# Optimization experiments

Measured on AMD Instinct MI355X. Metric: run time of the kernel, lower is better.

Reference implementation:

```python
import jax, jax.numpy as jnp
import numpy as np


def setup_inputs() -> dict:
    key = jax.random.key(0)
    ks = jax.random.split(key, 5)
    B, Lq, Lkv, HQ, H, D, S, BS = 1, 256, 4096, 32, 2, 128, 16, 64
    q = jax.random.normal(ks[0], (B, Lq, HQ, D), jnp.float32)
    k = jax.random.normal(ks[1], (B, Lkv, H, D), jnp.float32)
    v = jax.random.normal(ks[2], (B, Lkv, H, D), jnp.float32)
    w = jax.random.uniform(ks[3], (B, Lq, HQ, S), jnp.float32)
    block_indices = jax.random.randint(ks[4], (B, Lq, H, S), 0, Lkv // BS).astype(jnp.int32)
    return {"q": q, "k": k, "v": v, "w": w, "block_indices": block_indices, "block_size": BS}


def reference(q, k, v, w, block_indices, block_size):
    # q: (B, Lq, HQ, D); k,v: (B, Lkv, H, D); w: (B, Lq, HQ, num_weights);
    # block_indices: (B, Lq, H, S) int32, entries < 0 are skipped.
    B, Lq, HQ, D = q.shape
    H = k.shape[2]
    S = block_indices.shape[-1]
    G = HQ // H  # query heads per kv head
    nb = k.shape[1] // block_size
    sm_scale = 1.0 / (D ** 0.5)  # default scale in the kernel

    # Reshape KV into blocks: (B, H, nb, BS, D)
    kb = k.reshape(B, nb, block_size, H, D).transpose(0, 3, 1, 2, 4)
    vb = v.reshape(B, nb, block_size, H, D).transpose(0, 3, 1, 2, 4)

    idx = block_indices.transpose(0, 2, 1, 3)  # (B, H, Lq, S)
    valid = idx >= 0
    idx = jnp.maximum(idx, 0)

    # Gather selected blocks per (batch, kv_head): -> (B, H, Lq, S, BS, D)
    gather = jax.vmap(jax.vmap(lambda blocks, ind: blocks[ind]))
    kg = gather(kb, idx)
    vg = gather(vb, idx)

    # Group query heads by kv head: (B, H, Lq, G, D)
    qh = q.reshape(B, Lq, H, G, D).transpose(0, 2, 1, 3, 4)

    # Per-block scores and per-block softmax over the BS keys (axis u)
    scores = jnp.einsum('bhlgd,bhlsud->bhlgsu', qh, kg) * sm_scale
    p = jax.nn.softmax(scores, axis=-1)

    # Per-(head, block) learned weight; only first S weights of w are used.
    wh = w[..., :S].reshape(B, Lq, H, G, S).transpose(0, 2, 1, 3, 4)  # (B,H,Lq,G,S)
    coef = wh * valid[:, :, :, None, :].astype(p.dtype)
    p = p * coef[..., None]

    o = jnp.einsum('bhlgsu,bhlsud->bhlgd', p, vg)  # (B, H, Lq, G, D)
    return o.transpose(0, 2, 1, 3, 4).reshape(B, Lq, HQ, D)
```

## Files before the change

kernel.cpp:

```cpp
#include <hip/hip_runtime.h>
#include <hip/hip_bf16.h>


namespace {

constexpr int kLq = 256, kHQ = 32, kH = 2, kG = 16, kD = 128, kS = 16;
constexpr int kNB = 64;
constexpr float kScaleLog2e = 0.08838834764831845f * 1.4426950408889634f;

constexpr int kKPackN = kH * kNB * 16 * 64;
constexpr int kPStr   = 72;
constexpr int kSStr   = 136;

typedef short s16x8 __attribute__((ext_vector_type(8)));
typedef float f32x4 __attribute__((ext_vector_type(4)));

union U32BF2 { unsigned int u; __hip_bfloat162 h; };
union FragU  { uint4 u; s16x8 v; };

static __device__ inline unsigned int pk_bf16(float a, float b) {
    U32BF2 z; z.h = __float22bfloat162_rn(make_float2(a, b));
    return z.u;
}

__global__ __launch_bounds__(256)
void pack_kv(const float* __restrict__ k, const float* __restrict__ v,
             uint4* __restrict__ kp, uint4* __restrict__ vp)
{
    __shared__ unsigned short S_s[32 * kSStr];

    const int bid  = blockIdx.x;
    const int isV  = bid & 1;
    const int half = (bid >> 1) & 1;
    const int blk  = (bid >> 2) & 63;
    const int h    = bid >> 8;
    const int t    = threadIdx.x;
    const int lane = t & 63, n = lane & 15, quad = lane >> 4;
    const int wv   = t >> 6;

    {
        const float* src = (isV ? v : k) +
            ((size_t)(blk * 64 + half * 32) * kH + h) * kD;
        const int r0 = t >> 5, c4 = (t & 31) << 2;
        #pragma unroll
        for (int p = 0; p < 4; ++p) {
            const int r = p * 8 + r0;
            const float4 f = *(const float4*)(src + (size_t)r * (kH * kD) + c4);
            *(unsigned int*)&S_s[r * kSStr + c4]     = pk_bf16(f.x, f.y);
            *(unsigned int*)&S_s[r * kSStr + c4 + 2] = pk_bf16(f.z, f.w);
        }
    }
    __syncthreads();

    const size_t obase = (size_t)(h * 64 + blk) * 16 * 64;
    if (!isV) {
        #pragma unroll
        for (int rep = 0; rep < 2; ++rep) {
            const int cl    = wv * 2 + rep;
            const int t_loc = cl >> 2, st = cl & 3;
            const int c     = (2 * half + t_loc) * 4 + st;
            const int u_loc = t_loc * 16 + n;
            kp[obase + (size_t)c * 64 + lane] =
                *(const uint4*)&S_s[u_loc * kSStr + st * 32 + quad * 8];
        }
    } else {
        #pragma unroll
        for (int rep = 0; rep < 2; ++rep) {
            const int dt = wv * 2 + rep;
            const int c  = dt * 2 + half;
            const int d  = dt * 16 + n;
            unsigned short s[8];
            #pragma unroll
            for (int j = 0; j < 8; ++j) s[j] = S_s[(quad * 8 + j) * kSStr + d];
            uint4 val;
            val.x = s[0] | ((unsigned)s[1] << 16);
            val.y = s[2] | ((unsigned)s[3] << 16);
            val.z = s[4] | ((unsigned)s[5] << 16);
            val.w = s[6] | ((unsigned)s[7] << 16);
            vp[obase + (size_t)c * 64 + lane] = val;
        }
    }
}

__global__ __launch_bounds__(512, 4)
void hsa_main(const float* __restrict__ q, const float* __restrict__ w,
              const int* __restrict__ bidx, const uint4* __restrict__ kp,
              const uint4* __restrict__ vp, float* __restrict__ out)
{
    __shared__ __align__(16) float smem[8192];

    const int bid  = blockIdx.x;
    const int l    = bid >> 1;
    const int h    = bid & 1;
    const int tid  = threadIdx.x;
    const int wave = tid >> 6;
    const int lane = tid & 63;
    const int n    = lane & 15;
    const int quad = lane >> 4;

    s16x8 qf[4];
    {
        const float* qb = q + ((size_t)l * kHQ + h * kG + n) * kD + quad * 8;
        #pragma unroll
        for (int st = 0; st < 4; ++st) {
            const float4 f0 = *(const float4*)(qb + st * 32);
            const float4 f1 = *(const float4*)(qb + st * 32 + 4);
            union { s16x8 v; unsigned int u[4]; } z;
            z.u[0] = pk_bf16(f0.x, f0.y); z.u[1] = pk_bf16(f0.z, f0.w);
            z.u[2] = pk_bf16(f1.x, f1.y); z.u[3] = pk_bf16(f1.z, f1.w);
            qf[st] = z.v;
        }
    }

    int   base2[2];
    float wval2[2];
    #pragma unroll
    for (int j = 0; j < 2; ++j) {
        const int s  = wave * 2 + j;
        const int bi = bidx[(size_t)(l * kH + h) * kS + s];
        wval2[j] = (bi < 0) ? 0.f : w[((size_t)l * kHQ + h * kG + n) * kS + s];
        base2[j] = (h * kNB + max(bi, 0)) * 1024;
    }

    unsigned short* Pw = (unsigned short*)smem + wave * (kG * kPStr);

    FragU kA[4], kB[4], vr[4];
    #pragma unroll
    for (int st = 0; st < 4; ++st) kA[st].u = kp[base2[0] + (0 * 4 + st) * 64 + lane];
    #pragma unroll
    for (int st = 0; st < 4; ++st) kB[st].u = kp[base2[0] + (1 * 4 + st) * 64 + lane];
    #pragma unroll
    for (int i = 0; i < 4; ++i)    vr[i].u  = vp[base2[0] + i * 64 + lane];
    __builtin_amdgcn_sched_barrier(0);

    f32x4 oacc[8];
    #pragma unroll
    for (int dt = 0; dt < 8; ++dt) oacc[dt] = (f32x4){0.f, 0.f, 0.f, 0.f};

    #pragma unroll
    for (int jb = 0; jb < 2; ++jb) {
        float part = 0.f;
        #pragma unroll
        for (int t = 0; t < 4; ++t) {
            FragU* cur = (t & 1) ? kB : kA;
            f32x4 sc = {0.f, 0.f, 0.f, 0.f};
            #pragma unroll
            for (int st = 0; st < 4; ++st)
                sc = __builtin_amdgcn_mfma_f32_16x16x32_bf16(cur[st].v, qf[st], sc, 0, 0, 0);

            if (t < 2) {
                #pragma unroll
                for (int st = 0; st < 4; ++st)
                    cur[st].u = kp[base2[jb] + ((t + 2) * 4 + st) * 64 + lane];
            } else if (jb == 0) {
                #pragma unroll
                for (int st = 0; st < 4; ++st)
                    cur[st].u = kp[base2[1] + ((t - 2) * 4 + st) * 64 + lane];
            }
            __builtin_amdgcn_sched_barrier(0);

            #pragma unroll
            for (int r = 0; r < 4; ++r) {
                sc[r] = exp2f(sc[r] * kScaleLog2e);
                part += sc[r];
            }
            const unsigned long long pq =
                ((unsigned long long)pk_bf16(sc[2], sc[3]) << 32) | pk_bf16(sc[0], sc[1]);
            *(unsigned long long*)&Pw[n * kPStr + t * 16 + quad * 4] = pq;
        }

        part += __shfl_xor(part, 16);
        part += __shfl_xor(part, 32);
        const float coef = wval2[jb] / part;

        const s16x8 bf0 = *(const s16x8*)&Pw[n * kPStr + quad * 8];
        const s16x8 bf1 = *(const s16x8*)&Pw[n * kPStr + 32 + quad * 8];

        const f32x4 zero = {0.f, 0.f, 0.f, 0.f};
        #pragma unroll
        for (int vg = 0; vg < 4; ++vg) {
            const int dt0 = vg * 2;
            f32x4 p0 = __builtin_amdgcn_mfma_f32_16x16x32_bf16(vr[0].v, bf0, zero, 0, 0, 0);
            p0       = __builtin_amdgcn_mfma_f32_16x16x32_bf16(vr[1].v, bf1, p0,   0, 0, 0);
            f32x4 p1 = __builtin_amdgcn_mfma_f32_16x16x32_bf16(vr[2].v, bf0, zero, 0, 0, 0);
            p1       = __builtin_amdgcn_mfma_f32_16x16x32_bf16(vr[3].v, bf1, p1,   0, 0, 0);

            if (vg < 3) {
                #pragma unroll
                for (int i = 0; i < 4; ++i)
                    vr[i].u = vp[base2[jb] + ((vg + 1) * 4 + i) * 64 + lane];
            } else if (jb == 0) {
                #pragma unroll
                for (int i = 0; i < 4; ++i)
                    vr[i].u = vp[base2[1] + i * 64 + lane];
            }
            __builtin_amdgcn_sched_barrier(0);

            #pragma unroll
            for (int r = 0; r < 4; ++r) {
                oacc[dt0 + 0][r] = fmaf(coef, p0[r], oacc[dt0 + 0][r]);
                oacc[dt0 + 1][r] = fmaf(coef, p1[r], oacc[dt0 + 1][r]);
            }
        }
    }

    __syncthreads();
    float* epi = smem;

    if (wave >= 4) {
        #pragma unroll
        for (int dt = 0; dt < 8; ++dt)
            *(f32x4*)&epi[(wave - 4) * 2048 + dt * 256 + lane * 4] = oacc[dt];
    }
    __syncthreads();
    if (wave < 4) {
        #pragma unroll
        for (int dt = 0; dt < 8; ++dt) {
            const f32x4 o = *(const f32x4*)&epi[wave * 2048 + dt * 256 + lane * 4];
            #pragma unroll
            for (int r = 0; r < 4; ++r) oacc[dt][r] += o[r];
        }
    }
    __syncthreads();
    if (wave == 2 || wave == 3) {
        #pragma unroll
        for (int dt = 0; dt < 8; ++dt)
            *(f32x4*)&epi[(wave - 2) * 2048 + dt * 256 + lane * 4] = oacc[dt];
    }
    __syncthreads();
    if (wave < 2) {
        #pragma unroll
        for (int dt = 0; dt < 8; ++dt) {
            const f32x4 o = *(const f32x4*)&epi[wave * 2048 + dt * 256 + lane * 4];
            #pragma unroll
            for (int r = 0; r < 4; ++r) oacc[dt][r] += o[r];
        }
    }
    __syncthreads();
    if (wave == 1) {
        #pragma unroll
        for (int dt = 0; dt < 8; ++dt)
            *(f32x4*)&epi[dt * 256 + lane * 4] = oacc[dt];
    }
    __syncthreads();
    if (wave == 0) {
        float* ob = out + ((size_t)l * kHQ + h * kG + n) * kD;
        #pragma unroll
        for (int dt = 0; dt < 8; ++dt) {
            const f32x4 o = *(const f32x4*)&epi[dt * 256 + lane * 4];
            float4 val;
            #pragma unroll
            for (int r = 0; r < 4; ++r) (&val.x)[r] = oacc[dt][r] + o[r];
            *(float4*)(ob + dt * 16 + quad * 4) = val;
        }
    }
}

}

extern "C" void kernel_launch(void* const* d_in, const int* in_sizes, int n_in,
                              void* d_out, int out_size, void* d_ws, size_t ws_size,
                              hipStream_t stream)
{
    const float* q    = (const float*)d_in[0];
    const float* k    = (const float*)d_in[1];
    const float* v    = (const float*)d_in[2];
    const float* w    = (const float*)d_in[3];
    const int*   bidx = (const int*)d_in[4];
    float* out = (float*)d_out;

    uint4* kp = (uint4*)d_ws;
    uint4* vp = (uint4*)((char*)d_ws + (size_t)kKPackN * 16);

    pack_kv<<<dim3(512), dim3(256), 0, stream>>>(k, v, kp, vp);
    hsa_main<<<dim3(kLq * kH), dim3(512), 0, stream>>>(q, w, bidx, kp, vp, out);
}
```

Before: 89.02 us.

## Interleave two KV blocks' score phases and stage Q fragments in LDS

Each wave now computes QK scores for both of its selected blocks in interleaved order with separate K register buffers, and writes P into two LDS tiles. The PV phases then run back to back. Q fragments move from registers into LDS, which frees VGPRs but adds LDS reads before every MFMA. Shared memory grows to about 68 KB per block, which may cut the number of resident blocks below the launch-bound target of 4.

Result: no change. 88.81 us (-0.2%).

```diff
diff --git a/kernel.cpp b/kernel.cpp
--- a/kernel.cpp
+++ b/kernel.cpp
@@ -11,6 +11,9 @@
 constexpr int kKPackN = kH * kNB * 16 * 64;
 constexpr int kPStr   = 72;
 constexpr int kSStr   = 136;
+
+constexpr int kQOff = 0;
+constexpr int kPOff = 32768;
 
 typedef short s16x8 __attribute__((ext_vector_type(8)));
 typedef float f32x4 __attribute__((ext_vector_type(4)));
@@ -87,7 +90,7 @@
               const int* __restrict__ bidx, const uint4* __restrict__ kp,
               const uint4* __restrict__ vp, float* __restrict__ out)
 {
-    __shared__ __align__(16) float smem[8192];
+    __shared__ __align__(16) unsigned char smem[69632];
 
     const int bid  = blockIdx.x;
     const int l    = bid >> 1;
@@ -98,85 +101,108 @@
     const int n    = lane & 15;
     const int quad = lane >> 4;
 
-    s16x8 qf[4];
+    unsigned char* qlds = smem + kQOff + wave * 4096 + lane * 16;
     {
         const float* qb = q + ((size_t)l * kHQ + h * kG + n) * kD + quad * 8;
         #pragma unroll
         for (int st = 0; st < 4; ++st) {
             const float4 f0 = *(const float4*)(qb + st * 32);
             const float4 f1 = *(const float4*)(qb + st * 32 + 4);
-            union { s16x8 v; unsigned int u[4]; } z;
-            z.u[0] = pk_bf16(f0.x, f0.y); z.u[1] = pk_bf16(f0.z, f0.w);
-            z.u[2] = pk_bf16(f1.x, f1.y); z.u[3] = pk_bf16(f1.z, f1.w);
-            qf[st] = z.v;
-        }
-    }
-
-    int   base2[2];
-    float wval2[2];
-    #pragma unroll
-    for (int j = 0; j < 2; ++j) {
-        const int s  = wave * 2 + j;
-        const int bi = bidx[(size_t)(l * kH + h) * kS + s];
-        wval2[j] = (bi < 0) ? 0.f : w[((size_t)l * kHQ + h * kG + n) * kS + s];
-        base2[j] = (h * kNB + max(bi, 0)) * 1024;
-    }
-
-    unsigned short* Pw = (unsigned short*)smem + wave * (kG * kPStr);
+            uint4 z;
+            z.x = pk_bf16(f0.x, f0.y); z.y = pk_bf16(f0.z, f0.w);
+            z.z = pk_bf16(f1.x, f1.y); z.w = pk_bf16(f1.z, f1.w);
+            *(uint4*)(qlds + st * 1024) = z;
+        }
+    }
+
+    int   baseA, baseB;
+    float wvalA, wvalB;
+    {
+        const int sA = wave * 2, sB = wave * 2 + 1;
+        const int biA = bidx[(size_t)(l * kH + h) * kS + sA];
+        const int biB = bidx[(size_t)(l * kH + h) * kS + sB];
+        wvalA = (biA < 0) ? 0.f : w[((size_t)l * kHQ + h * kG + n) * kS + sA];
+        wvalB = (biB < 0) ? 0.f : w[((size_t)l * kHQ + h * kG + n) * kS + sB];
+        baseA = (h * kNB + max(biA, 0)) * 1024;
+        baseB = (h * kNB + max(biB, 0)) * 1024;
+    }
+
+    unsigned short* PA = (unsigned short*)(smem + kPOff + wave * 4608);
+    unsigned short* PB = PA + kG * kPStr;
 
     FragU kA[4], kB[4], vr[4];
     #pragma unroll
-    for (int st = 0; st < 4; ++st) kA[st].u = kp[base2[0] + (0 * 4 + st) * 64 + lane];
-    #pragma unroll
-    for (int st = 0; st < 4; ++st) kB[st].u = kp[base2[0] + (1 * 4 + st) * 64 + lane];
-    #pragma unroll
-    for (int i = 0; i < 4; ++i)    vr[i].u  = vp[base2[0] + i * 64 + lane];
+    for (int st = 0; st < 4; ++st) kA[st].u = kp[baseA + st * 64 + lane];
+    #pragma unroll
+    for (int st = 0; st < 4; ++st) kB[st].u = kp[baseB + st * 64 + lane];
+    #pragma unroll
+    for (int i = 0; i < 4; ++i)    vr[i].u  = vp[baseA + i * 64 + lane];
     __builtin_amdgcn_sched_barrier(0);
 
     f32x4 oacc[8];
     #pragma unroll
     for (int dt = 0; dt < 8; ++dt) oacc[dt] = (f32x4){0.f, 0.f, 0.f, 0.f};
 
-    #pragma unroll
-    for (int jb = 0; jb < 2; ++jb) {
-        float part = 0.f;
-        #pragma unroll
-        for (int t = 0; t < 4; ++t) {
-            FragU* cur = (t & 1) ? kB : kA;
+    float partA = 0.f, partB = 0.f;
+    #pragma unroll
+    for (int t = 0; t < 4; ++t) {
+        {
             f32x4 sc = {0.f, 0.f, 0.f, 0.f};
             #pragma unroll
-            for (int st = 0; st < 4; ++st)
-                sc = __builtin_amdgcn_mfma_f32_16x16x32_bf16(cur[st].v, qf[st], sc, 0, 0, 0);
-
-            if (t < 2) {
+            for (int st = 0; st < 4; ++st) {
+                const s16x8 aq = *(const s16x8*)(qlds + st * 1024);
+                sc = __builtin_amdgcn_mfma_f32_16x16x32_bf16(kA[st].v, aq, sc, 0, 0, 0);
+            }
+            if (t < 3) {
                 #pragma unroll
                 for (int st = 0; st < 4; ++st)
-                    cur[st].u = kp[base2[jb] + ((t + 2) * 4 + st) * 64 + lane];
-            } else if (jb == 0) {
-                #pragma unroll
-                for (int st = 0; st < 4; ++st)
-                    cur[st].u = kp[base2[1] + ((t - 2) * 4 + st) * 64 + lane];
+                    kA[st].u = kp[baseA + ((t + 1) * 4 + st) * 64 + lane];
             }
             __builtin_amdgcn_sched_barrier(0);
-
             #pragma unroll
             for (int r = 0; r < 4; ++r) {
                 sc[r] = exp2f(sc[r] * kScaleLog2e);
-                part += sc[r];
+                partA += sc[r];
             }
             const unsigned long long pq =
                 ((unsigned long long)pk_bf16(sc[2], sc[3]) << 32) | pk_bf16(sc[0], sc[1]);
-            *(unsigned long long*)&Pw[n * kPStr + t * 16 + quad * 4] = pq;
-        }
-
-        part += __shfl_xor(part, 16);
-        part += __shfl_xor(part, 32);
-        const float coef = wval2[jb] / part;
-
-        const s16x8 bf0 = *(const s16x8*)&Pw[n * kPStr + quad * 8];
-        const s16x8 bf1 = *(const s16x8*)&Pw[n * kPStr + 32 + quad * 8];
-
-        const f32x4 zero = {0.f, 0.f, 0.f, 0.f};
+            *(unsigned long long*)&PA[n * kPStr + t * 16 + quad * 4] = pq;
+        }
+        {
+            f32x4 sc = {0.f, 0.f, 0.f, 0.f};
+            #pragma unroll
+            for (int st = 0; st < 4; ++st) {
+                const s16x8 aq = *(const s16x8*)(qlds + st * 1024);
+                sc = __builtin_amdgcn_mfma_f32_16x16x32_bf16(kB[st].v, aq, sc, 0, 0, 0);
+            }
+            if (t < 3) {
+                #pragma unroll
+                for (int st = 0; st < 4; ++st)
+                    kB[st].u = kp[baseB + ((t + 1) * 4 + st) * 64 + lane];
+            }
+            __builtin_amdgcn_sched_barrier(0);
+            #pragma unroll
+            for (int r = 0; r < 4; ++r) {
+                sc[r] = exp2f(sc[r] * kScaleLog2e);
+                partB += sc[r];
+            }
+            const unsigned long long pq =
+                ((unsigned long long)pk_bf16(sc[2], sc[3]) << 32) | pk_bf16(sc[0], sc[1]);
+            *(unsigned long long*)&PB[n * kPStr + t * 16 + quad * 4] = pq;
+        }
+    }
+
+    partA += __shfl_xor(partA, 16);
+    partA += __shfl_xor(partA, 32);
+    partB += __shfl_xor(partB, 16);
+    partB += __shfl_xor(partB, 32);
+    const float coefA = wvalA / partA;
+    const float coefB = wvalB / partB;
+
+    const f32x4 zero = {0.f, 0.f, 0.f, 0.f};
+    {
+        const s16x8 bf0 = *(const s16x8*)&PA[n * kPStr + quad * 8];
+        const s16x8 bf1 = *(const s16x8*)&PA[n * kPStr + 32 + quad * 8];
         #pragma unroll
         for (int vg = 0; vg < 4; ++vg) {
             const int dt0 = vg * 2;
@@ -184,28 +210,49 @@
             p0       = __builtin_amdgcn_mfma_f32_16x16x32_bf16(vr[1].v, bf1, p0,   0, 0, 0);
             f32x4 p1 = __builtin_amdgcn_mfma_f32_16x16x32_bf16(vr[2].v, bf0, zero, 0, 0, 0);
             p1       = __builtin_amdgcn_mfma_f32_16x16x32_bf16(vr[3].v, bf1, p1,   0, 0, 0);
-
             if (vg < 3) {
                 #pragma unroll
                 for (int i = 0; i < 4; ++i)
-                    vr[i].u = vp[base2[jb] + ((vg + 1) * 4 + i) * 64 + lane];
-            } else if (jb == 0) {
+                    vr[i].u = vp[baseA + ((vg + 1) * 4 + i) * 64 + lane];
+            } else {
                 #pragma unroll
                 for (int i = 0; i < 4; ++i)
-                    vr[i].u = vp[base2[1] + i * 64 + lane];
+                    vr[i].u = vp[baseB + i * 64 + lane];
             }
             __builtin_amdgcn_sched_barrier(0);
-
             #pragma unroll
             for (int r = 0; r < 4; ++r) {
-                oacc[dt0 + 0][r] = fmaf(coef, p0[r], oacc[dt0 + 0][r]);
-                oacc[dt0 + 1][r] = fmaf(coef, p1[r], oacc[dt0 + 1][r]);
-            }
-        }
-    }
-
-    __syncthreads();
-    float* epi = smem;
+                oacc[dt0 + 0][r] = fmaf(coefA, p0[r], oacc[dt0 + 0][r]);
+                oacc[dt0 + 1][r] = fmaf(coefA, p1[r], oacc[dt0 + 1][r]);
+            }
+        }
+    }
+    {
+        const s16x8 bf0 = *(const s16x8*)&PB[n * kPStr + quad * 8];
+        const s16x8 bf1 = *(const s16x8*)&PB[n * kPStr + 32 + quad * 8];
+        #pragma unroll
+        for (int vg = 0; vg < 4; ++vg) {
+            const int dt0 = vg * 2;
+            f32x4 p0 = __builtin_amdgcn_mfma_f32_16x16x32_bf16(vr[0].v, bf0, zero, 0, 0, 0);
+            p0       = __builtin_amdgcn_mfma_f32_16x16x32_bf16(vr[1].v, bf1, p0,   0, 0, 0);
+            f32x4 p1 = __builtin_amdgcn_mfma_f32_16x16x32_bf16(vr[2].v, bf0, zero, 0, 0, 0);
+            p1       = __builtin_amdgcn_mfma_f32_16x16x32_bf16(vr[3].v, bf1, p1,   0, 0, 0);
+            if (vg < 3) {
+                #pragma unroll
+                for (int i = 0; i < 4; ++i)
+                    vr[i].u = vp[baseB + ((vg + 1) * 4 + i) * 64 + lane];
+            }
+            __builtin_amdgcn_sched_barrier(0);
+            #pragma unroll
+            for (int r = 0; r < 4; ++r) {
+                oacc[dt0 + 0][r] = fmaf(coefB, p0[r], oacc[dt0 + 0][r]);
+                oacc[dt0 + 1][r] = fmaf(coefB, p1[r], oacc[dt0 + 1][r]);
+            }
+        }
+    }
+
+    __syncthreads();
+    float* epi = (float*)(smem + kQOff);
 
     if (wave >= 4) {
         #pragma unroll
```

## Halve waves per block, four KV blocks per wave, Q fragments in LDS

Applied to the files above, without the earlier changes.

Drops the main kernel from 512 to 256 threads per block, so each wave now processes four selected KV blocks instead of two, and the cross-wave reduction loses one stage. The Q fragments are written to shared memory and re-read before each MFMA instead of being held in registers. A single K register buffer replaces the double buffer, freeing registers so the launch bound can request five blocks per CU. The cost is less parallelism per block, more sequential work per wave, extra LDS reads per MFMA, and less K prefetch depth.

Result: slower. 94.94 us (+6.7%).

```diff
diff --git a/kernel.cpp b/kernel.cpp
--- a/kernel.cpp
+++ b/kernel.cpp
@@ -11,6 +11,9 @@
 constexpr int kKPackN = kH * kNB * 16 * 64;
 constexpr int kPStr   = 72;
 constexpr int kSStr   = 136;
+
+constexpr int kQOff = 0;
+constexpr int kPOff = 4096;
 
 typedef short s16x8 __attribute__((ext_vector_type(8)));
 typedef float f32x4 __attribute__((ext_vector_type(4)));
@@ -82,12 +85,12 @@
     }
 }
 
-__global__ __launch_bounds__(512, 4)
+__global__ __launch_bounds__(256, 5)
 void hsa_main(const float* __restrict__ q, const float* __restrict__ w,
               const int* __restrict__ bidx, const uint4* __restrict__ kp,
               const uint4* __restrict__ vp, float* __restrict__ out)
 {
-    __shared__ __align__(16) float smem[8192];
+    __shared__ __align__(16) unsigned char smem[16384];
 
     const int bid  = blockIdx.x;
     const int l    = bid >> 1;
@@ -98,39 +101,37 @@
     const int n    = lane & 15;
     const int quad = lane >> 4;
 
-    s16x8 qf[4];
+    unsigned char* qlds = smem + kQOff + lane * 16;
     {
         const float* qb = q + ((size_t)l * kHQ + h * kG + n) * kD + quad * 8;
         #pragma unroll
         for (int st = 0; st < 4; ++st) {
             const float4 f0 = *(const float4*)(qb + st * 32);
             const float4 f1 = *(const float4*)(qb + st * 32 + 4);
-            union { s16x8 v; unsigned int u[4]; } z;
-            z.u[0] = pk_bf16(f0.x, f0.y); z.u[1] = pk_bf16(f0.z, f0.w);
-            z.u[2] = pk_bf16(f1.x, f1.y); z.u[3] = pk_bf16(f1.z, f1.w);
-            qf[st] = z.v;
-        }
-    }
-
-    int   base2[2];
-    float wval2[2];
-    #pragma unroll
-    for (int j = 0; j < 2; ++j) {
-        const int s  = wave * 2 + j;
+            uint4 z;
+            z.x = pk_bf16(f0.x, f0.y); z.y = pk_bf16(f0.z, f0.w);
+            z.z = pk_bf16(f1.x, f1.y); z.w = pk_bf16(f1.z, f1.w);
+            *(uint4*)(qlds + st * 1024) = z;
+        }
+    }
+
+    int   base4[4];
+    float wval4[4];
+    #pragma unroll
+    for (int j = 0; j < 4; ++j) {
+        const int s  = wave * 4 + j;
         const int bi = bidx[(size_t)(l * kH + h) * kS + s];
-        wval2[j] = (bi < 0) ? 0.f : w[((size_t)l * kHQ + h * kG + n) * kS + s];
-        base2[j] = (h * kNB + max(bi, 0)) * 1024;
-    }
-
-    unsigned short* Pw = (unsigned short*)smem + wave * (kG * kPStr);
-
-    FragU kA[4], kB[4], vr[4];
-    #pragma unroll
-    for (int st = 0; st < 4; ++st) kA[st].u = kp[base2[0] + (0 * 4 + st) * 64 + lane];
-    #pragma unroll
-    for (int st = 0; st < 4; ++st) kB[st].u = kp[base2[0] + (1 * 4 + st) * 64 + lane];
-    #pragma unroll
-    for (int i = 0; i < 4; ++i)    vr[i].u  = vp[base2[0] + i * 64 + lane];
+        wval4[j] = (bi < 0) ? 0.f : w[((size_t)l * kHQ + h * kG + n) * kS + s];
+        base4[j] = (h * kNB + max(bi, 0)) * 1024;
+    }
+
+    unsigned short* Pw = (unsigned short*)(smem + kPOff + wave * 2304);
+
+    FragU kr[4], vr[4];
+    #pragma unroll
+    for (int st = 0; st < 4; ++st) kr[st].u = kp[base4[0] + st * 64 + lane];
+    #pragma unroll
+    for (int i = 0; i < 4; ++i)    vr[i].u  = vp[base4[0] + i * 64 + lane];
     __builtin_amdgcn_sched_barrier(0);
 
     f32x4 oacc[8];
@@ -138,24 +139,24 @@
     for (int dt = 0; dt < 8; ++dt) oacc[dt] = (f32x4){0.f, 0.f, 0.f, 0.f};
 
     #pragma unroll
-    for (int jb = 0; jb < 2; ++jb) {
+    for (int j = 0; j < 4; ++j) {
         float part = 0.f;
         #pragma unroll
         for (int t = 0; t < 4; ++t) {
-            FragU* cur = (t & 1) ? kB : kA;
             f32x4 sc = {0.f, 0.f, 0.f, 0.f};
             #pragma unroll
-            for (int st = 0; st < 4; ++st)
-                sc = __builtin_amdgcn_mfma_f32_16x16x32_bf16(cur[st].v, qf[st], sc, 0, 0, 0);
-
-            if (t < 2) {
+            for (int st = 0; st < 4; ++st) {
+                const s16x8 aq = *(const s16x8*)(qlds + st * 1024);
+                sc = __builtin_amdgcn_mfma_f32_16x16x32_bf16(kr[st].v, aq, sc, 0, 0, 0);
+            }
+            if (t < 3) {
                 #pragma unroll
                 for (int st = 0; st < 4; ++st)
-                    cur[st].u = kp[base2[jb] + ((t + 2) * 4 + st) * 64 + lane];
-            } else if (jb == 0) {
+                    kr[st].u = kp[base4[j] + ((t + 1) * 4 + st) * 64 + lane];
+            } else if (j < 3) {
                 #pragma unroll
                 for (int st = 0; st < 4; ++st)
-                    cur[st].u = kp[base2[1] + ((t - 2) * 4 + st) * 64 + lane];
+                    kr[st].u = kp[base4[j + 1] + st * 64 + lane];
             }
             __builtin_amdgcn_sched_barrier(0);
 
@@ -171,7 +172,7 @@
 
         part += __shfl_xor(part, 16);
         part += __shfl_xor(part, 32);
-        const float coef = wval2[jb] / part;
+        const float coef = wval4[j] / part;
 
         const s16x8 bf0 = *(const s16x8*)&Pw[n * kPStr + quad * 8];
         const s16x8 bf1 = *(const s16x8*)&Pw[n * kPStr + 32 + quad * 8];
@@ -184,15 +185,14 @@
             p0       = __builtin_amdgcn_mfma_f32_16x16x32_bf16(vr[1].v, bf1, p0,   0, 0, 0);
             f32x4 p1 = __builtin_amdgcn_mfma_f32_16x16x32_bf16(vr[2].v, bf0, zero, 0, 0, 0);
             p1       = __builtin_amdgcn_mfma_f32_16x16x32_bf16(vr[3].v, bf1, p1,   0, 0, 0);
-
             if (vg < 3) {
                 #pragma unroll
                 for (int i = 0; i < 4; ++i)
-                    vr[i].u = vp[base2[jb] + ((vg + 1) * 4 + i) * 64 + lane];
-            } else if (jb == 0) {
+                    vr[i].u = vp[base4[j] + ((vg + 1) * 4 + i) * 64 + lane];
+            } else if (j < 3) {
                 #pragma unroll
                 for (int i = 0; i < 4; ++i)
-                    vr[i].u = vp[base2[1] + i * 64 + lane];
+                    vr[i].u = vp[base4[j + 1] + i * 64 + lane];
             }
             __builtin_amdgcn_sched_barrier(0);
 
@@ -205,24 +205,9 @@
     }
 
     __syncthreads();
-    float* epi = smem;
-
-    if (wave >= 4) {
-        #pragma unroll
-        for (int dt = 0; dt < 8; ++dt)
-            *(f32x4*)&epi[(wave - 4) * 2048 + dt * 256 + lane * 4] = oacc[dt];
-    }
-    __syncthreads();
-    if (wave < 4) {
-        #pragma unroll
-        for (int dt = 0; dt < 8; ++dt) {
-            const f32x4 o = *(const f32x4*)&epi[wave * 2048 + dt * 256 + lane * 4];
-            #pragma unroll
-            for (int r = 0; r < 4; ++r) oacc[dt][r] += o[r];
-        }
-    }
-    __syncthreads();
-    if (wave == 2 || wave == 3) {
+    float* epi = (float*)smem;
+
+    if (wave >= 2) {
         #pragma unroll
         for (int dt = 0; dt < 8; ++dt)
             *(f32x4*)&epi[(wave - 2) * 2048 + dt * 256 + lane * 4] = oacc[dt];
@@ -273,5 +258,5 @@
     uint4* vp = (uint4*)((char*)d_ws + (size_t)kKPackN * 16);
 
     pack_kv<<<dim3(512), dim3(256), 0, stream>>>(k, v, kp, vp);
-    hsa_main<<<dim3(kLq * kH), dim3(512), 0, stream>>>(q, w, bidx, kp, vp, out);
-}
+    hsa_main<<<dim3(kLq * kH), dim3(256), 0, stream>>>(q, w, bidx, kp, vp, out);
+}
```
